# Kernel tuning notes

Hardware: AMD Instinct MI355X
Metric: run time of the kernel (lower is better)

## Reference

```python
import jax, jax.numpy as jnp
import numpy as np
import math

N, CH, T, S = 32, 64, 2048, 77  # batch*heads, per-head channels, query len, encoder len

def setup_inputs() -> dict:
    key = jax.random.key(0)
    k1, k2 = jax.random.split(key)
    qkv = jax.random.normal(k1, (N, 3 * CH, T), dtype=jnp.float32)
    encoder_kv = jax.random.normal(k2, (N, 2 * CH, S), dtype=jnp.float32)
    attn_mask = jnp.zeros((1, T, S + T), dtype=jnp.float32)
    return {"qkv": qkv, "encoder_kv": encoder_kv, "attn_mask": attn_mask}

def reference(qkv, encoder_kv, attn_mask):
    ch = qkv.shape[1] // 3
    q, k, v = jnp.split(qkv, 3, axis=1)          # each [N, ch, T]
    ek, ev = jnp.split(encoder_kv, 2, axis=1)    # each [N, ch, S]
    k = jnp.concatenate([ek, k], axis=-1)        # [N, ch, S+T]
    v = jnp.concatenate([ev, v], axis=-1)
    scale = 1.0 / math.sqrt(math.sqrt(ch))
    weight = jnp.einsum('bct,bcs->bts', q * scale, k * scale)  # [N, T, S+T]
    weight = weight.astype(jnp.float32) + attn_mask
    weight = jax.nn.softmax(weight, axis=-1).astype(v.dtype)
    return jnp.einsum('bts,bcs->bct', weight, v)  # [N, ch, T]
```

## Files before the change

### kernel.cpp

```cpp
#include <hip/hip_runtime.h>


typedef __attribute__((ext_vector_type(8))) __bf16 bf16x8;
typedef __attribute__((ext_vector_type(8))) unsigned short u16x8;
typedef __attribute__((ext_vector_type(4))) float f32x4;
typedef float f32x4a __attribute__((ext_vector_type(4))) __attribute__((aligned(4)));
typedef __attribute__((ext_vector_type(4))) unsigned u32x4;
typedef __attribute__((ext_vector_type(2))) unsigned u32x2;

#define L2E  1.44269504089f
#define NEGM (-23.0830936f)

static __device__ __forceinline__ unsigned short f2bf(float f) {
    unsigned u = __builtin_bit_cast(unsigned, f);
    u += 0x7fffu + ((u >> 16) & 1u);
    return (unsigned short)(u >> 16);
}
static __device__ __forceinline__ unsigned pack_bf16(float a, float b) {
    return (unsigned)f2bf(a) | ((unsigned)f2bf(b) << 16);
}

__global__ __launch_bounds__(256) void prep_k(const float* __restrict__ qkv,
                                              const float* __restrict__ ekv,
                                              unsigned short* __restrict__ kws) {
    __shared__ float tile[64][65];
    int b = blockIdx.x;
    int tid = threadIdx.x;
    int mode, n, t0;
    if (b < 1024) { mode = 1; n = b >> 5;          t0 = (b & 31) << 6; }
    else          { mode = 2; n = (b - 1024) >> 1; t0 = ((b - 1024) & 1) << 6; }

    const float* src;
    size_t srow;
    int tmax = 64;
    if (mode == 1) { src = qkv + (size_t)n * 192 * 2048 + (size_t)64 * 2048 + t0; srow = 2048; }
    else           { src = ekv + (size_t)n * 128 * 77 + t0; srow = 77;
                     tmax = 77 - t0; if (tmax > 64) tmax = 64; }

    #pragma unroll
    for (int i = 0; i < 4; ++i) {
        int idx = tid + (i << 8);
        int c  = idx >> 4;
        int t4 = (idx & 15) << 2;
        const float* p = src + (size_t)c * srow + t4;
        float v0, v1, v2, v3;
        if (mode == 1) {
            f32x4 v = *(const f32x4*)p;
            v0 = v.x; v1 = v.y; v2 = v.z; v3 = v.w;
        } else {
            v0 = (t4 + 0 < tmax) ? p[0] : 0.f;
            v1 = (t4 + 1 < tmax) ? p[1] : 0.f;
            v2 = (t4 + 2 < tmax) ? p[2] : 0.f;
            v3 = (t4 + 3 < tmax) ? p[3] : 0.f;
        }
        tile[t4 + 0][c] = v0;
        tile[t4 + 1][c] = v1;
        tile[t4 + 2][c] = v2;
        tile[t4 + 3][c] = v3;
    }
    __syncthreads();
    #pragma unroll
    for (int i = 0; i < 4; ++i) {
        int idx = tid + (i << 8);
        int row = idx >> 4;
        int c4  = (idx & 15) << 2;
        if (mode == 2 && row >= tmax) continue;
        u32x2 pk;
        pk.x = pack_bf16(tile[row][c4 + 0], tile[row][c4 + 1]);
        pk.y = pack_bf16(tile[row][c4 + 2], tile[row][c4 + 3]);
        unsigned short* dst;
        if (mode == 1) dst = kws + ((size_t)n * 2176 + 77 + t0 + row) * 64;
        else           dst = kws + ((size_t)n * 2176 + t0 + row) * 64;
        *(u32x2*)(dst + c4) = pk;
    }
}

__global__ __launch_bounds__(256) void prep_v(const float* __restrict__ qkv,
                                              const float* __restrict__ ekv,
                                              unsigned short* __restrict__ vws) {
    int b = blockIdx.x;
    int n = b >> 6, c = b & 63;
    const float* v  = qkv + (size_t)n * 192 * 2048 + (size_t)(128 + c) * 2048;
    const float* ev = ekv + (size_t)n * 128 * 77 + (size_t)(64 + c) * 77;
    unsigned short* dst = vws + ((size_t)n * 64 + c) * 2176;
    for (int u = threadIdx.x; u < 544; u += 256) {
        int s = u << 2;
        float f[4];
        if (u >= 20 && u <= 530) {
            f32x4a x = *(const f32x4a*)(v + s - 77);
            f[0] = x.x; f[1] = x.y; f[2] = x.z; f[3] = x.w;
        } else {
            #pragma unroll
            for (int k = 0; k < 4; ++k) {
                int sk = s + k;
                f[k] = (sk < 77) ? ev[sk] : ((sk < 2125) ? v[sk - 77] : 0.f);
            }
        }
        u32x2 pk; pk.x = pack_bf16(f[0], f[1]); pk.y = pack_bf16(f[2], f[3]);
        *(u32x2*)(dst + s) = pk;
    }
}

__global__ __launch_bounds__(256, 2) void flash_attn(
        const float* __restrict__ qkv,
        const unsigned short* __restrict__ kws,
        const unsigned short* __restrict__ vws,
        const float* __restrict__ mask,
        float* __restrict__ out) {
    __shared__ alignas(16) unsigned short k_lds[64 * 72];
    __shared__ alignas(16) unsigned short v_lds[64 * 72];
    __shared__ alignas(16) unsigned short p_lds[4][32 * 72];

    const int n    = blockIdx.y;
    const int t0   = blockIdx.x << 7;
    const int tid  = threadIdx.x;
    const int wave = tid >> 6;
    const int lane = tid & 63;
    const int q    = lane >> 4;
    const int l16  = lane & 15;
    const int tc0  = t0 + (wave << 5) + l16;
    const int tc1  = tc0 + 16;

    bf16x8 qf[2][2];
    #pragma unroll
    for (int h = 0; h < 2; ++h) {
        const float* qsrc = qkv + (size_t)n * 192 * 2048 + (h ? tc1 : tc0);
        u16x8 a0, a1;
        #pragma unroll
        for (int j = 0; j < 8; ++j) {
            a0[j] = f2bf(qsrc[(size_t)((q << 3) + j) * 2048] * 0.125f);
            a1[j] = f2bf(qsrc[(size_t)(32 + (q << 3) + j) * 2048] * 0.125f);
        }
        qf[h][0] = __builtin_bit_cast(bf16x8, a0);
        qf[h][1] = __builtin_bit_cast(bf16x8, a1);
    }

    const unsigned short* kg = kws + (size_t)n * 2176 * 64;
    const unsigned short* vg = vws + (size_t)n * 64 * 2176;
    const float* mrow0 = mask + (size_t)tc0 * 2125;
    const float* mrow1 = mask + (size_t)tc1 * 2125;
    unsigned short* const pw0 = p_lds[wave] + (size_t)l16 * 72;
    unsigned short* const pw1 = p_lds[wave] + (size_t)(16 + l16) * 72;

    f32x4 of[2][4] = {};
    float lsum0 = 0.f, lsum1 = 0.f;

    for (int ks = 0; ks < 34; ++ks) {
        const int s0 = ks << 6;
        __syncthreads();
        #pragma unroll
        for (int i = 0; i < 2; ++i) {
            int f   = tid + (i << 8);
            int row = f >> 3, ch = f & 7;
            u32x4 kd = *(const u32x4*)(kg + (size_t)(s0 + row) * 64 + (ch << 3));
            *(u32x4*)(k_lds + row * 72 + (ch << 3)) = kd;
            u32x4 vd = *(const u32x4*)(vg + (size_t)row * 2176 + s0 + (ch << 3));
            *(u32x4*)(v_lds + row * 72 + (ch << 3)) = vd;
        }
        __syncthreads();

        const bool tail = (s0 + 64 > 2125);
        #pragma unroll
        for (int sm = 0; sm < 4; ++sm) {
            const unsigned short* kp = k_lds + (size_t)((sm << 4) + l16) * 72 + (q << 3);
            bf16x8 ak0 = *(const bf16x8*)(kp);
            bf16x8 ak1 = *(const bf16x8*)(kp + 32);
            int sbase  = s0 + (sm << 4) + (q << 2);
            int sclamp = sbase > 2121 ? 2121 : sbase;
            #pragma unroll
            for (int h = 0; h < 2; ++h) {
                f32x4 acc = {};
                acc = __builtin_amdgcn_mfma_f32_16x16x32_bf16(ak0, qf[h][0], acc, 0, 0, 0);
                acc = __builtin_amdgcn_mfma_f32_16x16x32_bf16(ak1, qf[h][1], acc, 0, 0, 0);
                f32x4a mr = *(const f32x4a*)((h ? mrow1 : mrow0) + sclamp);
                acc += f32x4{mr.x, mr.y, mr.z, mr.w};
                if (tail) {
                    #pragma unroll
                    for (int j = 0; j < 4; ++j)
                        if (sbase + j >= 2125) acc[j] = -1e30f;
                }
                float p0 = __builtin_amdgcn_exp2f(__builtin_fmaf(acc[0], L2E, NEGM));
                float p1 = __builtin_amdgcn_exp2f(__builtin_fmaf(acc[1], L2E, NEGM));
                float p2 = __builtin_amdgcn_exp2f(__builtin_fmaf(acc[2], L2E, NEGM));
                float p3 = __builtin_amdgcn_exp2f(__builtin_fmaf(acc[3], L2E, NEGM));
                if (h) lsum1 += (p0 + p1) + (p2 + p3);
                else   lsum0 += (p0 + p1) + (p2 + p3);
                u32x2 pk; pk.x = pack_bf16(p0, p1); pk.y = pack_bf16(p2, p3);
                *(u32x2*)((h ? pw1 : pw0) + (sm << 4) + (q << 2)) = pk;
            }
        }

        bf16x8 bp00 = *(const bf16x8*)(pw0 + (q << 3));
        bf16x8 bp01 = *(const bf16x8*)(pw0 + (q << 3) + 32);
        bf16x8 bp10 = *(const bf16x8*)(pw1 + (q << 3));
        bf16x8 bp11 = *(const bf16x8*)(pw1 + (q << 3) + 32);
        #pragma unroll
        for (int cm = 0; cm < 4; ++cm) {
            const unsigned short* vp = v_lds + (size_t)((cm << 4) + l16) * 72 + (q << 3);
            bf16x8 av0 = *(const bf16x8*)(vp);
            bf16x8 av1 = *(const bf16x8*)(vp + 32);
            of[0][cm] = __builtin_amdgcn_mfma_f32_16x16x32_bf16(av0, bp00, of[0][cm], 0, 0, 0);
            of[0][cm] = __builtin_amdgcn_mfma_f32_16x16x32_bf16(av1, bp01, of[0][cm], 0, 0, 0);
            of[1][cm] = __builtin_amdgcn_mfma_f32_16x16x32_bf16(av0, bp10, of[1][cm], 0, 0, 0);
            of[1][cm] = __builtin_amdgcn_mfma_f32_16x16x32_bf16(av1, bp11, of[1][cm], 0, 0, 0);
        }
    }

    lsum0 += __shfl_xor(lsum0, 16, 64);
    lsum0 += __shfl_xor(lsum0, 32, 64);
    lsum1 += __shfl_xor(lsum1, 16, 64);
    lsum1 += __shfl_xor(lsum1, 32, 64);
    float inv0 = 1.0f / lsum0, inv1 = 1.0f / lsum1;
    #pragma unroll
    for (int cm = 0; cm < 4; ++cm)
        #pragma unroll
        for (int j = 0; j < 4; ++j) {
            int c = (cm << 4) + (q << 2) + j;
            float* o = out + ((size_t)n * 64 + c) * 2048;
            o[tc0] = of[0][cm][j] * inv0;
            o[tc1] = of[1][cm][j] * inv1;
        }
}

extern "C" void kernel_launch(void* const* d_in, const int* in_sizes, int n_in,
                              void* d_out, int out_size, void* d_ws, size_t ws_size,
                              hipStream_t stream) {
    const float* qkv  = (const float*)d_in[0];
    const float* ekv  = (const float*)d_in[1];
    const float* mask = (const float*)d_in[2];
    float* out = (float*)d_out;

    unsigned short* kws = (unsigned short*)d_ws;
    unsigned short* vws = kws + (size_t)32 * 2176 * 64;

    prep_k<<<1088, 256, 0, stream>>>(qkv, ekv, kws);
    prep_v<<<2048, 256, 0, stream>>>(qkv, ekv, vws);
    dim3 grid(16, 32);
    flash_attn<<<grid, 256, 0, stream>>>(qkv, kws, vws, mask, out);
}
```

Before: 184.5 us.

## Register-prefetch next K/V tile and mask; merge prep kernels into one launch

```diff
diff --git a/kernel.cpp b/kernel.cpp
--- a/kernel.cpp
+++ b/kernel.cpp
@@ -20,12 +20,39 @@
     return (unsigned)f2bf(a) | ((unsigned)f2bf(b) << 16);
 }
 
-__global__ __launch_bounds__(256) void prep_k(const float* __restrict__ qkv,
-                                              const float* __restrict__ ekv,
-                                              unsigned short* __restrict__ kws) {
-    __shared__ float tile[64][65];
+__global__ __launch_bounds__(256) void prep_all(const float* __restrict__ qkv,
+                                                const float* __restrict__ ekv,
+                                                unsigned short* __restrict__ kws,
+                                                unsigned short* __restrict__ vws) {
     int b = blockIdx.x;
     int tid = threadIdx.x;
+
+    if (b >= 1088) {
+        int bb = b - 1088;
+        int n = bb >> 6, c = bb & 63;
+        const float* v  = qkv + (size_t)n * 192 * 2048 + (size_t)(128 + c) * 2048;
+        const float* ev = ekv + (size_t)n * 128 * 77 + (size_t)(64 + c) * 77;
+        unsigned short* dst = vws + ((size_t)n * 64 + c) * 2176;
+        for (int u = tid; u < 544; u += 256) {
+            int s = u << 2;
+            float f[4];
+            if (u >= 20 && u <= 530) {
+                f32x4a x = *(const f32x4a*)(v + s - 77);
+                f[0] = x.x; f[1] = x.y; f[2] = x.z; f[3] = x.w;
+            } else {
+                #pragma unroll
+                for (int k = 0; k < 4; ++k) {
+                    int sk = s + k;
+                    f[k] = (sk < 77) ? ev[sk] : ((sk < 2125) ? v[sk - 77] : 0.f);
+                }
+            }
+            u32x2 pk; pk.x = pack_bf16(f[0], f[1]); pk.y = pack_bf16(f[2], f[3]);
+            *(u32x2*)(dst + s) = pk;
+        }
+        return;
+    }
+
+    __shared__ float tile[64][65];
     int mode, n, t0;
     if (b < 1024) { mode = 1; n = b >> 5;          t0 = (b & 31) << 6; }
     else          { mode = 2; n = (b - 1024) >> 1; t0 = ((b - 1024) & 1) << 6; }
@@ -75,32 +102,6 @@
     }
 }
 
-__global__ __launch_bounds__(256) void prep_v(const float* __restrict__ qkv,
-                                              const float* __restrict__ ekv,
-                                              unsigned short* __restrict__ vws) {
-    int b = blockIdx.x;
-    int n = b >> 6, c = b & 63;
-    const float* v  = qkv + (size_t)n * 192 * 2048 + (size_t)(128 + c) * 2048;
-    const float* ev = ekv + (size_t)n * 128 * 77 + (size_t)(64 + c) * 77;
-    unsigned short* dst = vws + ((size_t)n * 64 + c) * 2176;
-    for (int u = threadIdx.x; u < 544; u += 256) {
-        int s = u << 2;
-        float f[4];
-        if (u >= 20 && u <= 530) {
-            f32x4a x = *(const f32x4a*)(v + s - 77);
-            f[0] = x.x; f[1] = x.y; f[2] = x.z; f[3] = x.w;
-        } else {
-            #pragma unroll
-            for (int k = 0; k < 4; ++k) {
-                int sk = s + k;
-                f[k] = (sk < 77) ? ev[sk] : ((sk < 2125) ? v[sk - 77] : 0.f);
-            }
-        }
-        u32x2 pk; pk.x = pack_bf16(f[0], f[1]); pk.y = pack_bf16(f[2], f[3]);
-        *(u32x2*)(dst + s) = pk;
-    }
-}
-
 __global__ __launch_bounds__(256, 2) void flash_attn(
         const float* __restrict__ qkv,
         const unsigned short* __restrict__ kws,
@@ -142,22 +143,45 @@
     unsigned short* const pw0 = p_lds[wave] + (size_t)l16 * 72;
     unsigned short* const pw1 = p_lds[wave] + (size_t)(16 + l16) * 72;
 
+    const int srow0 = tid >> 3,        sch = (tid & 7) << 3;
+    const int srow1 = (tid + 256) >> 3;
+
     f32x4 of[2][4] = {};
     float lsum0 = 0.f, lsum1 = 0.f;
+
+    u32x4 kreg[2], vreg[2];
+    f32x4 mreg[4][2];
+
+    auto issue_kv = [&](int s0) {
+        kreg[0] = *(const u32x4*)(kg + (size_t)(s0 + srow0) * 64 + sch);
+        vreg[0] = *(const u32x4*)(vg + (size_t)srow0 * 2176 + s0 + sch);
+        kreg[1] = *(const u32x4*)(kg + (size_t)(s0 + srow1) * 64 + sch);
+        vreg[1] = *(const u32x4*)(vg + (size_t)srow1 * 2176 + s0 + sch);
+    };
+    auto issue_mask = [&](int s0) {
+        #pragma unroll
+        for (int sm = 0; sm < 4; ++sm) {
+            int sbase = s0 + (sm << 4) + (q << 2);
+            int sclamp = sbase > 2121 ? 2121 : sbase;
+            f32x4a m0 = *(const f32x4a*)(mrow0 + sclamp);
+            f32x4a m1 = *(const f32x4a*)(mrow1 + sclamp);
+            mreg[sm][0] = f32x4{m0.x, m0.y, m0.z, m0.w};
+            mreg[sm][1] = f32x4{m1.x, m1.y, m1.z, m1.w};
+        }
+    };
+
+    issue_kv(0);
+    issue_mask(0);
 
     for (int ks = 0; ks < 34; ++ks) {
         const int s0 = ks << 6;
         __syncthreads();
-        #pragma unroll
-        for (int i = 0; i < 2; ++i) {
-            int f   = tid + (i << 8);
-            int row = f >> 3, ch = f & 7;
-            u32x4 kd = *(const u32x4*)(kg + (size_t)(s0 + row) * 64 + (ch << 3));
-            *(u32x4*)(k_lds + row * 72 + (ch << 3)) = kd;
-            u32x4 vd = *(const u32x4*)(vg + (size_t)row * 2176 + s0 + (ch << 3));
-            *(u32x4*)(v_lds + row * 72 + (ch << 3)) = vd;
-        }
+        *(u32x4*)(k_lds + srow0 * 72 + sch) = kreg[0];
+        *(u32x4*)(v_lds + srow0 * 72 + sch) = vreg[0];
+        *(u32x4*)(k_lds + srow1 * 72 + sch) = kreg[1];
+        *(u32x4*)(v_lds + srow1 * 72 + sch) = vreg[1];
         __syncthreads();
+        if (ks < 33) issue_kv(s0 + 64);
 
         const bool tail = (s0 + 64 > 2125);
         #pragma unroll
@@ -165,15 +189,13 @@
             const unsigned short* kp = k_lds + (size_t)((sm << 4) + l16) * 72 + (q << 3);
             bf16x8 ak0 = *(const bf16x8*)(kp);
             bf16x8 ak1 = *(const bf16x8*)(kp + 32);
-            int sbase  = s0 + (sm << 4) + (q << 2);
-            int sclamp = sbase > 2121 ? 2121 : sbase;
+            int sbase = s0 + (sm << 4) + (q << 2);
             #pragma unroll
             for (int h = 0; h < 2; ++h) {
                 f32x4 acc = {};
                 acc = __builtin_amdgcn_mfma_f32_16x16x32_bf16(ak0, qf[h][0], acc, 0, 0, 0);
                 acc = __builtin_amdgcn_mfma_f32_16x16x32_bf16(ak1, qf[h][1], acc, 0, 0, 0);
-                f32x4a mr = *(const f32x4a*)((h ? mrow1 : mrow0) + sclamp);
-                acc += f32x4{mr.x, mr.y, mr.z, mr.w};
+                acc += mreg[sm][h];
                 if (tail) {
                     #pragma unroll
                     for (int j = 0; j < 4; ++j)
@@ -189,6 +211,7 @@
                 *(u32x2*)((h ? pw1 : pw0) + (sm << 4) + (q << 2)) = pk;
             }
         }
+        if (ks < 33) issue_mask(s0 + 64);
 
         bf16x8 bp00 = *(const bf16x8*)(pw0 + (q << 3));
         bf16x8 bp01 = *(const bf16x8*)(pw0 + (q << 3) + 32);
@@ -233,8 +256,7 @@
     unsigned short* kws = (unsigned short*)d_ws;
     unsigned short* vws = kws + (size_t)32 * 2176 * 64;
 
-    prep_k<<<1088, 256, 0, stream>>>(qkv, ekv, kws);
-    prep_v<<<2048, 256, 0, stream>>>(qkv, ekv, vws);
+    prep_all<<<3136, 256, 0, stream>>>(qkv, ekv, kws, vws);
     dim3 grid(16, 32);
     flash_attn<<<grid, 256, 0, stream>>>(qkv, kws, vws, mask, out);
 }
```

Result: faster. 177.0 us (-4.1%).
